# Kernel tuning notes

Measured on AMD Instinct MI355X. Metric: run time of the kernel, lower is better.

Reference implementation:

```python
import jax, jax.numpy as jnp
import numpy as np


def setup_inputs() -> dict:
    key = jax.random.key(0)
    kc, kh, kx, kwx, kwh = jax.random.split(key, 5)
    B, T, D, H = 64, 512, 1024, 1024
    c0 = jax.random.normal(kc, (B, H), dtype=jnp.float32)
    h0 = jax.random.normal(kh, (B, H), dtype=jnp.float32)
    xs = jax.random.normal(kx, (B, T, D), dtype=jnp.float32)
    # fan-in scaled init like lecun_normal (flax default)
    Wx = jax.random.normal(kwx, (D, 4 * H), dtype=jnp.float32) / np.sqrt(D)
    Wh = jax.random.normal(kwh, (H, 4 * H), dtype=jnp.float32) / np.sqrt(H)
    b = jnp.zeros((4 * H,), dtype=jnp.float32)
    return {"c0": c0, "h0": h0, "xs": xs, "Wx": Wx, "Wh": Wh, "b": b}


def _lstm(c0, h0, xs, Wx, Wh, b):
    # Batch the input-to-hidden projection across all timesteps (compute-dense GEMM)
    xproj = jnp.einsum('btd,dh->tbh', xs, Wx)  # [T, B, 4H], time-major for scan

    def step(carry, xp):
        c, h = carry
        gates = xp + h @ Wh + b                # [B, 4H]
        i, f, g, o = jnp.split(gates, 4, axis=-1)  # flax gate order: i, f, g, o
        new_c = jax.nn.sigmoid(f) * c + jax.nn.sigmoid(i) * jnp.tanh(g)
        new_h = jax.nn.sigmoid(o) * jnp.tanh(new_c)
        return (new_c, new_h), new_h

    (cT, hT), ys = jax.lax.scan(step, (c0, h0), xproj)
    return (cT, hT), jnp.transpose(ys, (1, 0, 2))  # ys back to [B, T, H]


def reference(c0, h0, xs, Wx, Wh, b):
    return _lstm(c0, h0, xs, Wx, Wh, b)
```

## Files before the change

### kernel.cpp

```cpp
#include <hip/hip_runtime.h>


typedef _Float16 half8 __attribute__((ext_vector_type(8)));
typedef float floatx4 __attribute__((ext_vector_type(4)));

#define T_DIM 512
#define B_DIM 64
#define H_DIM 1024
#define FOURH 4096

__device__ __forceinline__ void gll16(const void* g, void* l) {
  __builtin_amdgcn_global_load_lds(
      (const __attribute__((address_space(1))) unsigned int*)g,
      (__attribute__((address_space(3))) unsigned int*)l, 16, 0, 0);
}

__device__ __forceinline__ float sigm(float x) { return 1.f / (1.f + __expf(-x)); }
__device__ __forceinline__ float tanhfast(float x) { return 1.f - 2.f / (__expf(2.f * x) + 1.f); }

__global__ void prep_ew(const float* __restrict__ xs, const float* __restrict__ h0,
                        _Float16* __restrict__ xs16, _Float16* __restrict__ hb0,
                        int* __restrict__ flags) {
  long gid = (long)blockIdx.x * blockDim.x + threadIdx.x;
  if (gid < 4194304) {
    const float4* p = (const float4*)xs + gid * 2;
    float4 u = p[0], w = p[1];
    half8 o;
    o[0] = (_Float16)u.x; o[1] = (_Float16)u.y; o[2] = (_Float16)u.z; o[3] = (_Float16)u.w;
    o[4] = (_Float16)w.x; o[5] = (_Float16)w.y; o[6] = (_Float16)w.z; o[7] = (_Float16)w.w;
    *(half8*)(xs16 + gid * 8) = o;
  } else if (gid < 4202496) {
    long j = gid - 4194304;
    const float4* p = (const float4*)h0 + j * 2;
    float4 u = p[0], w = p[1];
    half8 o;
    o[0] = (_Float16)u.x; o[1] = (_Float16)u.y; o[2] = (_Float16)u.z; o[3] = (_Float16)u.w;
    o[4] = (_Float16)w.x; o[5] = (_Float16)w.y; o[6] = (_Float16)w.z; o[7] = (_Float16)w.w;
    *(half8*)(hb0 + j * 8) = o;
  } else if (gid < 4202560) {
    flags[gid - 4202496] = 0;
  }
}

__global__ void transpose_k(const float* __restrict__ in, _Float16* __restrict__ outp) {
  __shared__ float s[32][33];
  int bx = blockIdx.x * 32, by = blockIdx.y * 32;
  int tx = threadIdx.x, ty = threadIdx.y;
#pragma unroll
  for (int k = 0; k < 32; k += 8)
    s[ty + k][tx] = in[(long)(by + ty + k) * 4096 + bx + tx];
  __syncthreads();
#pragma unroll
  for (int k = 0; k < 32; k += 8)
    outp[(long)(bx + ty + k) * 1024 + by + tx] = (_Float16)s[tx][ty + k];
}

__global__ __launch_bounds__(256) void gemm1(const _Float16* __restrict__ A,
                                             const _Float16* __restrict__ Bt,
                                             _Float16* __restrict__ C) {
  __shared__ _Float16 sA[4096], sB[4096];
  const int tid = threadIdx.x;
  const int w = tid >> 6, l = tid & 63, li = l & 15, q = l >> 4;
  const int wr = w >> 1, wc = w & 1;
  const int m0 = blockIdx.y * 128, n0 = blockIdx.x * 128;
  floatx4 acc[4][4] = {};
  const _Float16* gA0 = A + (long)(m0 + (w * 16 + li)) * 1024 + q * 8;
  const _Float16* gA1 = A + (long)(m0 + ((4 + w) * 16 + li)) * 1024 + q * 8;
  const _Float16* gB0 = Bt + (long)(n0 + (w * 16 + li)) * 1024 + q * 8;
  const _Float16* gB1 = Bt + (long)(n0 + ((4 + w) * 16 + li)) * 1024 + q * 8;
  _Float16* lA0 = sA + (w * 64) * 8;
  _Float16* lA1 = sA + (256 + w * 64) * 8;
  _Float16* lB0 = sB + (w * 64) * 8;
  _Float16* lB1 = sB + (256 + w * 64) * 8;
  for (int k0 = 0; k0 < 1024; k0 += 32) {
    __syncthreads();
    gll16(gA0 + k0, lA0);
    gll16(gA1 + k0, lA1);
    gll16(gB0 + k0, lB0);
    gll16(gB1 + k0, lB1);
    __syncthreads();
    half8 af[4], bf[4];
    const half8* pA = (const half8*)sA;
    const half8* pB = (const half8*)sB;
#pragma unroll
    for (int i = 0; i < 4; i++) af[i] = pA[(wr * 4 + i) * 64 + l];
#pragma unroll
    for (int j = 0; j < 4; j++) bf[j] = pB[(wc * 4 + j) * 64 + l];
#pragma unroll
    for (int i = 0; i < 4; i++)
#pragma unroll
      for (int j = 0; j < 4; j++)
        acc[i][j] = __builtin_amdgcn_mfma_f32_16x16x32_f16(af[i], bf[j], acc[i][j], 0, 0, 0);
  }
#pragma unroll
  for (int i = 0; i < 4; i++) {
#pragma unroll
    for (int r = 0; r < 4; r++) {
      int m = m0 + wr * 64 + i * 16 + q * 4 + r;
      long orow = (long)(m & 511) * 64 + (m >> 9);
#pragma unroll
      for (int j = 0; j < 4; j++) {
        int gn = n0 + wc * 64 + j * 16 + li;
        C[orow * 4096 + gn] = (_Float16)acc[i][j][r];
      }
    }
  }
}

__global__ __launch_bounds__(128, 1) void rec(const _Float16* __restrict__ xproj,
                                              const _Float16* __restrict__ Wht,
                                              const float* __restrict__ bias,
                                              const float* __restrict__ c0,
                                              _Float16* __restrict__ hbuf,
                                              int* __restrict__ flags,
                                              float* __restrict__ out) {
  __shared__ _Float16 sW[65536];
  __shared__ _Float16 sXp[4096];
  const int tid = threadIdx.x;
  const int wgid = blockIdx.x;
  const int v = tid >> 6;
  const int l = tid & 63, li = l & 15, q = l >> 4;
  const int ks = wgid * 16;

#pragma unroll 4
  for (int i = 0; i < 64; i++) {
    int c = i * 128 + tid;
    int g = c >> 11, kk = (c >> 6) & 31;
    gll16(Wht + (long)((g << 10) + ks + li) * 1024 + kk * 32 + q * 8, sW + (long)(c - l) * 8);
  }
  float creg[2][4];
#pragma unroll
  for (int a = 0; a < 2; a++)
#pragma unroll
    for (int r = 0; r < 4; r++)
      creg[a][r] = c0[((v * 2 + a) * 16 + q * 4 + r) * 1024 + ks + li];
  float bs[4];
#pragma unroll
  for (int g = 0; g < 4; g++) bs[g] = bias[(g << 10) + ks + li];
  __syncthreads();

  for (int t = 0; t < 512; t++) {
    for (;;) {
      int f = __hip_atomic_load(&flags[l], __ATOMIC_RELAXED, __HIP_MEMORY_SCOPE_AGENT);
      if (__all(f >= t)) break;
      __builtin_amdgcn_s_sleep(1);
    }
    __builtin_amdgcn_fence(__ATOMIC_ACQUIRE, "workgroup");

    const _Float16* xpt = xproj + (long)t * 262144;
#pragma unroll
    for (int i = 0; i < 4; i++) {
      int c = i * 128 + tid;
      int g = c >> 7, b = (c >> 1) & 63, hh = c & 1;
      gll16(xpt + (long)b * 4096 + (g << 10) + ks + hh * 8, sXp + (c - l) * 8);
    }

    const _Float16* h0p = hbuf + (long)t * 65536 + (long)((v * 2 + 0) * 16 + li) * 1024 + q * 8;
    const _Float16* h1p = hbuf + (long)t * 65536 + (long)((v * 2 + 1) * 16 + li) * 1024 + q * 8;
    floatx4 acc[2][4] = {};
    half8 ap0[4], ap1[4];
#pragma unroll
    for (int p = 0; p < 4; p++) {
      ap0[p] = *(const half8*)(h0p + p * 32);
      ap1[p] = *(const half8*)(h1p + p * 32);
    }
    const half8* pW = (const half8*)sW;
#pragma unroll
    for (int kk = 0; kk < 32; kk++) {
      half8 a0 = ap0[kk & 3], a1 = ap1[kk & 3];
#pragma unroll
      for (int g = 0; g < 4; g++) {
        half8 b = pW[((g * 32 + kk) << 6) + l];
        acc[0][g] = __builtin_amdgcn_mfma_f32_16x16x32_f16(a0, b, acc[0][g], 0, 0, 0);
        acc[1][g] = __builtin_amdgcn_mfma_f32_16x16x32_f16(a1, b, acc[1][g], 0, 0, 0);
      }
      if (kk < 28) {
        ap0[kk & 3] = *(const half8*)(h0p + (kk + 4) * 32);
        ap1[kk & 3] = *(const half8*)(h1p + (kk + 4) * 32);
      }
    }
    __syncthreads();

    _Float16* hnext = hbuf + (long)(t + 1) * 65536;
#pragma unroll
    for (int a = 0; a < 2; a++) {
#pragma unroll
      for (int r = 0; r < 4; r++) {
        int b = (v * 2 + a) * 16 + q * 4 + r;
        float gi = acc[a][0][r] + (float)sXp[((0 << 7) + b * 2 + (li >> 3)) * 8 + (li & 7)] + bs[0];
        float gf = acc[a][1][r] + (float)sXp[((1 << 7) + b * 2 + (li >> 3)) * 8 + (li & 7)] + bs[1];
        float gg = acc[a][2][r] + (float)sXp[((2 << 7) + b * 2 + (li >> 3)) * 8 + (li & 7)] + bs[2];
        float go = acc[a][3][r] + (float)sXp[((3 << 7) + b * 2 + (li >> 3)) * 8 + (li & 7)] + bs[3];
        float cN = sigm(gf) * creg[a][r] + sigm(gi) * tanhfast(gg);
        creg[a][r] = cN;
        float hN = sigm(go) * tanhfast(cN);
        unsigned short hu = __builtin_bit_cast(unsigned short, (_Float16)hN);
        __hip_atomic_store((unsigned short*)hnext + (long)b * 1024 + ks + li, hu,
                           __ATOMIC_RELAXED, __HIP_MEMORY_SCOPE_AGENT);
        out[131072 + (long)b * 524288 + (long)t * 1024 + ks + li] = hN;
        if (t == 511) {
          out[(long)b * 1024 + ks + li] = cN;
          out[65536 + (long)b * 1024 + ks + li] = hN;
        }
      }
    }
    __builtin_amdgcn_s_waitcnt(0);
    __syncthreads();
    if (tid == 0)
      __hip_atomic_store(&flags[wgid], t + 1, __ATOMIC_RELAXED, __HIP_MEMORY_SCOPE_AGENT);
  }
}

extern "C" void kernel_launch(void* const* d_in, const int* in_sizes, int n_in,
                              void* d_out, int out_size, void* d_ws, size_t ws_size,
                              hipStream_t stream) {
  const float* c0 = (const float*)d_in[0];
  const float* h0 = (const float*)d_in[1];
  const float* xs = (const float*)d_in[2];
  const float* Wx = (const float*)d_in[3];
  const float* Wh = (const float*)d_in[4];
  const float* bias = (const float*)d_in[5];
  float* out = (float*)d_out;

  char* ws = (char*)d_ws;
  size_t off = 0;
  _Float16* xs16 = (_Float16*)(ws + off); off += 67108864;
  _Float16* wxt  = (_Float16*)(ws + off); off += 8388608;
  _Float16* wht  = (_Float16*)(ws + off); off += 8388608;
  _Float16* xprj = (_Float16*)(ws + off); off += 268435456;
  _Float16* hbuf = (_Float16*)(ws + off); off += 67239936;
  int* flags     = (int*)(ws + off);      off += 256;
  if (ws_size < off) return;

  prep_ew<<<16417, 256, 0, stream>>>(xs, h0, xs16, hbuf, flags);
  transpose_k<<<dim3(128, 32), dim3(32, 8), 0, stream>>>(Wx, wxt);
  transpose_k<<<dim3(128, 32), dim3(32, 8), 0, stream>>>(Wh, wht);
  gemm1<<<dim3(32, 256), 256, 0, stream>>>(xs16, wxt, xprj);
  rec<<<64, 128, 0, stream>>>(xprj, wht, bias, c0, hbuf, flags, out);
}
```

Before: 6.253 ms.

## Split recurrent workgroup into per-wave batch slices with per-wave flags

The recurrent kernel now runs 256 threads per block, with each of four waves owning 16 batch rows instead of two waves owning 32. Each wave publishes its own completion flag, so the per-step __syncthreads barriers go away and consumers poll 256 flags. The xproj gate inputs are loaded straight into registers before the spin-wait, replacing the per-step LDS staging, and the output writes are moved after the flag store. This aims to shorten the per-step critical path of the serial recurrence. In exchange, the polling traffic on the flag array grows, and each wave now reads the whole 1024-wide h row from global memory.

```diff
diff --git a/kernel.cpp b/kernel.cpp
--- a/kernel.cpp
+++ b/kernel.cpp
@@ -3,11 +3,6 @@
 
 typedef _Float16 half8 __attribute__((ext_vector_type(8)));
 typedef float floatx4 __attribute__((ext_vector_type(4)));
-
-#define T_DIM 512
-#define B_DIM 64
-#define H_DIM 1024
-#define FOURH 4096
 
 __device__ __forceinline__ void gll16(const void* g, void* l) {
   __builtin_amdgcn_global_load_lds(
@@ -37,7 +32,7 @@
     o[0] = (_Float16)u.x; o[1] = (_Float16)u.y; o[2] = (_Float16)u.z; o[3] = (_Float16)u.w;
     o[4] = (_Float16)w.x; o[5] = (_Float16)w.y; o[6] = (_Float16)w.z; o[7] = (_Float16)w.w;
     *(half8*)(hb0 + j * 8) = o;
-  } else if (gid < 4202560) {
+  } else if (gid < 4202752) {
     flags[gid - 4202496] = 0;
   }
 }
@@ -107,7 +102,7 @@
   }
 }
 
-__global__ __launch_bounds__(128, 1) void rec(const _Float16* __restrict__ xproj,
+__global__ __launch_bounds__(256, 1) void rec(const _Float16* __restrict__ xproj,
                                               const _Float16* __restrict__ Wht,
                                               const float* __restrict__ bias,
                                               const float* __restrict__ c0,
@@ -115,7 +110,6 @@
                                               int* __restrict__ flags,
                                               float* __restrict__ out) {
   __shared__ _Float16 sW[65536];
-  __shared__ _Float16 sXp[4096];
   const int tid = threadIdx.x;
   const int wgid = blockIdx.x;
   const int v = tid >> 6;
@@ -123,91 +117,90 @@
   const int ks = wgid * 16;
 
 #pragma unroll 4
-  for (int i = 0; i < 64; i++) {
-    int c = i * 128 + tid;
+  for (int i = 0; i < 32; i++) {
+    int c = i * 256 + tid;
     int g = c >> 11, kk = (c >> 6) & 31;
-    gll16(Wht + (long)((g << 10) + ks + li) * 1024 + kk * 32 + q * 8, sW + (long)(c - l) * 8);
-  }
-  float creg[2][4];
-#pragma unroll
-  for (int a = 0; a < 2; a++)
-#pragma unroll
-    for (int r = 0; r < 4; r++)
-      creg[a][r] = c0[((v * 2 + a) * 16 + q * 4 + r) * 1024 + ks + li];
+    int cli = c & 15, cq = (c >> 4) & 3;
+    gll16(Wht + (long)((g << 10) + ks + cli) * 1024 + kk * 32 + cq * 8,
+          sW + (long)(c - l) * 8);
+  }
+  float creg[4];
+#pragma unroll
+  for (int r = 0; r < 4; r++)
+    creg[r] = c0[(long)(v * 16 + q * 4 + r) * 1024 + ks + li];
   float bs[4];
 #pragma unroll
   for (int g = 0; g < 4; g++) bs[g] = bias[(g << 10) + ks + li];
   __syncthreads();
 
+  const half8* pW = (const half8*)sW;
+  const int fbase = 4 * l;
+
   for (int t = 0; t < 512; t++) {
+    const _Float16* xpt = xproj + (long)t * 262144 + ks + li;
+    _Float16 xv[4][4];
+#pragma unroll
+    for (int g = 0; g < 4; g++)
+#pragma unroll
+      for (int r = 0; r < 4; r++)
+        xv[g][r] = xpt[(long)(v * 16 + q * 4 + r) * 4096 + (g << 10)];
+
     for (;;) {
-      int f = __hip_atomic_load(&flags[l], __ATOMIC_RELAXED, __HIP_MEMORY_SCOPE_AGENT);
-      if (__all(f >= t)) break;
+      int f0 = __hip_atomic_load(&flags[fbase + 0], __ATOMIC_RELAXED, __HIP_MEMORY_SCOPE_AGENT);
+      int f1 = __hip_atomic_load(&flags[fbase + 1], __ATOMIC_RELAXED, __HIP_MEMORY_SCOPE_AGENT);
+      int f2 = __hip_atomic_load(&flags[fbase + 2], __ATOMIC_RELAXED, __HIP_MEMORY_SCOPE_AGENT);
+      int f3 = __hip_atomic_load(&flags[fbase + 3], __ATOMIC_RELAXED, __HIP_MEMORY_SCOPE_AGENT);
+      int fm = min(min(f0, f1), min(f2, f3));
+      if (__all(fm >= t)) break;
       __builtin_amdgcn_s_sleep(1);
     }
     __builtin_amdgcn_fence(__ATOMIC_ACQUIRE, "workgroup");
 
-    const _Float16* xpt = xproj + (long)t * 262144;
-#pragma unroll
-    for (int i = 0; i < 4; i++) {
-      int c = i * 128 + tid;
-      int g = c >> 7, b = (c >> 1) & 63, hh = c & 1;
-      gll16(xpt + (long)b * 4096 + (g << 10) + ks + hh * 8, sXp + (c - l) * 8);
-    }
-
-    const _Float16* h0p = hbuf + (long)t * 65536 + (long)((v * 2 + 0) * 16 + li) * 1024 + q * 8;
-    const _Float16* h1p = hbuf + (long)t * 65536 + (long)((v * 2 + 1) * 16 + li) * 1024 + q * 8;
-    floatx4 acc[2][4] = {};
-    half8 ap0[4], ap1[4];
-#pragma unroll
-    for (int p = 0; p < 4; p++) {
-      ap0[p] = *(const half8*)(h0p + p * 32);
-      ap1[p] = *(const half8*)(h1p + p * 32);
-    }
-    const half8* pW = (const half8*)sW;
+    const _Float16* hrow = hbuf + (long)t * 65536 + (long)(v * 16 + li) * 1024 + q * 8;
+    floatx4 acc[4] = {};
+    half8 ap[8];
+#pragma unroll
+    for (int p = 0; p < 8; p++) ap[p] = *(const half8*)(hrow + p * 32);
 #pragma unroll
     for (int kk = 0; kk < 32; kk++) {
-      half8 a0 = ap0[kk & 3], a1 = ap1[kk & 3];
-#pragma unroll
-      for (int g = 0; g < 4; g++) {
-        half8 b = pW[((g * 32 + kk) << 6) + l];
-        acc[0][g] = __builtin_amdgcn_mfma_f32_16x16x32_f16(a0, b, acc[0][g], 0, 0, 0);
-        acc[1][g] = __builtin_amdgcn_mfma_f32_16x16x32_f16(a1, b, acc[1][g], 0, 0, 0);
+      half8 a = ap[kk & 7];
+#pragma unroll
+      for (int g = 0; g < 4; g++)
+        acc[g] = __builtin_amdgcn_mfma_f32_16x16x32_f16(a, pW[((g * 32 + kk) << 6) + l], acc[g], 0, 0, 0);
+      if (kk < 24) ap[kk & 7] = *(const half8*)(hrow + (kk + 8) * 32);
+    }
+
+    _Float16* hnext = hbuf + (long)(t + 1) * 65536;
+    float hval[4], cval[4];
+#pragma unroll
+    for (int r = 0; r < 4; r++) {
+      float gi = acc[0][r] + (float)xv[0][r] + bs[0];
+      float gf = acc[1][r] + (float)xv[1][r] + bs[1];
+      float gg = acc[2][r] + (float)xv[2][r] + bs[2];
+      float go = acc[3][r] + (float)xv[3][r] + bs[3];
+      float cN = sigm(gf) * creg[r] + sigm(gi) * tanhfast(gg);
+      creg[r] = cN;
+      cval[r] = cN;
+      float hN = sigm(go) * tanhfast(cN);
+      hval[r] = hN;
+      int b = v * 16 + q * 4 + r;
+      unsigned short hu = __builtin_bit_cast(unsigned short, (_Float16)hN);
+      __hip_atomic_store((unsigned short*)hnext + (long)b * 1024 + ks + li, hu,
+                         __ATOMIC_RELAXED, __HIP_MEMORY_SCOPE_AGENT);
+    }
+    __builtin_amdgcn_s_waitcnt(0);
+    if (l == 0)
+      __hip_atomic_store(&flags[4 * wgid + v], t + 1, __ATOMIC_RELAXED, __HIP_MEMORY_SCOPE_AGENT);
+
+#pragma unroll
+    for (int r = 0; r < 4; r++) {
+      int b = v * 16 + q * 4 + r;
+      out[131072 + (long)b * 524288 + (long)t * 1024 + ks + li] = hval[r];
+      if (t == 511) {
+        out[(long)b * 1024 + ks + li] = cval[r];
+        out[65536 + (long)b * 1024 + ks + li] = hval[r];
       }
-      if (kk < 28) {
-        ap0[kk & 3] = *(const half8*)(h0p + (kk + 4) * 32);
-        ap1[kk & 3] = *(const half8*)(h1p + (kk + 4) * 32);
-      }
-    }
-    __syncthreads();
-
-    _Float16* hnext = hbuf + (long)(t + 1) * 65536;
-#pragma unroll
-    for (int a = 0; a < 2; a++) {
-#pragma unroll
-      for (int r = 0; r < 4; r++) {
-        int b = (v * 2 + a) * 16 + q * 4 + r;
-        float gi = acc[a][0][r] + (float)sXp[((0 << 7) + b * 2 + (li >> 3)) * 8 + (li & 7)] + bs[0];
-        float gf = acc[a][1][r] + (float)sXp[((1 << 7) + b * 2 + (li >> 3)) * 8 + (li & 7)] + bs[1];
-        float gg = acc[a][2][r] + (float)sXp[((2 << 7) + b * 2 + (li >> 3)) * 8 + (li & 7)] + bs[2];
-        float go = acc[a][3][r] + (float)sXp[((3 << 7) + b * 2 + (li >> 3)) * 8 + (li & 7)] + bs[3];
-        float cN = sigm(gf) * creg[a][r] + sigm(gi) * tanhfast(gg);
-        creg[a][r] = cN;
-        float hN = sigm(go) * tanhfast(cN);
-        unsigned short hu = __builtin_bit_cast(unsigned short, (_Float16)hN);
-        __hip_atomic_store((unsigned short*)hnext + (long)b * 1024 + ks + li, hu,
-                           __ATOMIC_RELAXED, __HIP_MEMORY_SCOPE_AGENT);
-        out[131072 + (long)b * 524288 + (long)t * 1024 + ks + li] = hN;
-        if (t == 511) {
-          out[(long)b * 1024 + ks + li] = cN;
-          out[65536 + (long)b * 1024 + ks + li] = hN;
-        }
-      }
-    }
-    __builtin_amdgcn_s_waitcnt(0);
-    __syncthreads();
-    if (tid == 0)
-      __hip_atomic_store(&flags[wgid], t + 1, __ATOMIC_RELAXED, __HIP_MEMORY_SCOPE_AGENT);
+    }
   }
 }
 
@@ -229,12 +222,12 @@
   _Float16* wht  = (_Float16*)(ws + off); off += 8388608;
   _Float16* xprj = (_Float16*)(ws + off); off += 268435456;
   _Float16* hbuf = (_Float16*)(ws + off); off += 67239936;
-  int* flags     = (int*)(ws + off);      off += 256;
+  int* flags     = (int*)(ws + off);      off += 1024;
   if (ws_size < off) return;
 
   prep_ew<<<16417, 256, 0, stream>>>(xs, h0, xs16, hbuf, flags);
   transpose_k<<<dim3(128, 32), dim3(32, 8), 0, stream>>>(Wx, wxt);
   transpose_k<<<dim3(128, 32), dim3(32, 8), 0, stream>>>(Wh, wht);
   gemm1<<<dim3(32, 256), 256, 0, stream>>>(xs16, wxt, xprj);
-  rec<<<64, 128, 0, stream>>>(xprj, wht, bias, c0, hbuf, flags, out);
-}
+  rec<<<64, 256, 0, stream>>>(xprj, wht, bias, c0, hbuf, flags, out);
+}
```

Result: faster. 6.043 ms (-3.3%).
